# Kernel tuning notes

Measured on AMD Instinct MI355X. Metric: run time of the kernel, lower is better.

## Reference

```python
import jax, jax.numpy as jnp
import numpy as np

OUTPUT_DIM = 2
HIDDEN_DIM = 512
NUM_MODES = 6
PRED_LEN = 60
BATCH = 8192


def setup_inputs() -> dict:
    key = jax.random.key(0)
    ks = jax.random.split(key, 12)
    H, D, M = HIDDEN_DIM, OUTPUT_DIM, NUM_MODES
    s = 1.0 / np.sqrt(H)  # PyTorch default uniform(-1/sqrt(H), 1/sqrt(H))
    u = lambda k, shape: jax.random.uniform(k, shape, jnp.float32, -s, s)
    return {
        "social_features": jax.random.normal(ks[0], (BATCH, H), jnp.float32),
        "hidden": jax.random.normal(ks[1], (1, BATCH, H), jnp.float32),
        "cell": jax.random.normal(ks[2], (1, BATCH, H), jnp.float32),
        "w_ih": u(ks[3], (4 * H, D + H)),   # LSTM input->gates (i,f,g,o)
        "w_hh": u(ks[4], (4 * H, H)),       # LSTM hidden->gates
        "b_ih": u(ks[5], (4 * H,)),
        "b_hh": u(ks[6], (4 * H,)),
        "w_out": u(ks[7], (D * M, H)),      # output_layer
        "b_out": u(ks[8], (D * M,)),
        "w_mode": u(ks[9], (M, H)),         # mode_prob_layer
        "b_mode": u(ks[10], (M,)),
        "pred_len": PRED_LEN,
    }


def _decode(social_features, hidden, cell, w_ih, w_hh, b_ih, b_hh,
            w_out, b_out, w_mode, b_mode, pred_len):
    B = social_features.shape[0]
    H, D, M = HIDDEN_DIM, OUTPUT_DIM, NUM_MODES
    h0 = hidden[0]  # num_layers == 1
    c0 = cell[0]
    x0 = jnp.zeros((B, D), social_features.dtype)
    bias = b_ih + b_hh

    def step(carry, _):
        x, h, c = carry
        inp = jnp.concatenate([x, social_features], axis=-1)  # [B, D+H]
        gates = inp @ w_ih.T + h @ w_hh.T + bias              # [B, 4H]
        i, f, g, o = jnp.split(gates, 4, axis=-1)             # PyTorch gate order
        i = jax.nn.sigmoid(i)
        f = jax.nn.sigmoid(f)
        g = jnp.tanh(g)
        o = jax.nn.sigmoid(o)
        c_new = f * c + i * g
        h_new = o * jnp.tanh(c_new)
        pred = (h_new @ w_out.T + b_out).reshape(B, M, D)     # [B, M, D]
        mode_prob = jax.nn.softmax(h_new @ w_mode.T + b_mode, axis=-1)  # [B, M]
        x_next = pred[:, 0, :]
        return (x_next, h_new, c_new), (pred, mode_prob)

    _, (preds, probs) = jax.lax.scan(step, (x0, h0, c0), None, length=pred_len)
    # scan stacks on leading time axis -> move to batch-first
    predictions = jnp.transpose(preds, (1, 0, 2, 3))  # [B, T, M, D]
    mode_probs = jnp.transpose(probs, (1, 0, 2))      # [B, T, M]
    return predictions, mode_probs


def reference(social_features, hidden, cell, w_ih, w_hh, b_ih, b_hh,
              w_out, b_out, w_mode, b_mode, pred_len):
    return _decode(social_features, hidden, cell, w_ih, w_hh, b_ih, b_hh,
                   w_out, b_out, w_mode, b_mode, pred_len)
```

## Files before the change

kernel.cpp:

```cpp
#include <hip/hip_runtime.h>

#define H 512
#define BATCHN 8192
#define STEPS 60

#define WEFF_OFF   0u
#define WPLAIN_OFF 2097152u
#define WIHS_OFF   4194304u
#define WSM_OFF    6291456u
#define BSM_OFF    6324224u
#define BX1_OFF    6324352u
#define BX0_OFF    6332544u
#define HB0_OFF    8388608u
#define HB1_OFF    16777216u
#define CPACK_OFF  25165824u
#define SPACK_OFF  41943040u

typedef short s16x8 __attribute__((ext_vector_type(8)));
typedef float f32x4 __attribute__((ext_vector_type(4)));
typedef unsigned int u32x2 __attribute__((ext_vector_type(2)));
typedef unsigned int u32x4 __attribute__((ext_vector_type(4)));

__device__ inline unsigned f2bf(float f) {
  unsigned u = __builtin_bit_cast(unsigned, f);
  return (u + 0x7fffu + ((u >> 16) & 1u)) >> 16;
}
__device__ inline float bf2f(unsigned s) {
  return __builtin_bit_cast(float, s << 16);
}
__device__ inline float sigm(float x) {
  float e = __builtin_amdgcn_exp2f(-1.442695041f * x);
  return __builtin_amdgcn_rcpf(1.0f + e);
}
__device__ inline float tanh_(float x) {
  float e = __builtin_amdgcn_exp2f(2.885390082f * x);
  return 1.0f - 2.0f * __builtin_amdgcn_rcpf(1.0f + e);
}
__device__ inline f32x4 mfma16(s16x8 a, s16x8 b, f32x4 c) {
  return __builtin_amdgcn_mfma_f32_16x16x32_bf16(a, b, c, 0, 0, 0);
}
__device__ inline int haddr(int b, int k) {
  return b * 1024 + ((k * 2) ^ ((b & 7) << 4));
}

__global__ void pack_kernel(const float* __restrict__ w_ih, const float* __restrict__ w_hh,
                            const float* __restrict__ w_out, const float* __restrict__ b_out,
                            const float* __restrict__ w_mode, const float* __restrict__ b_mode,
                            unsigned char* __restrict__ ws) {
  unsigned idx = blockIdx.x * 256 + threadIdx.x;
  if (idx < 2097152u) {
    unsigned j = idx & 1048575u;
    bool eff = idx < 1048576u;
    unsigned e = j & 7u, lane = (j >> 3) & 63u, kb = (j >> 9) & 15u, T = j >> 13;
    unsigned i = lane & 15u;
    unsigned hcol = T * 4u + (i >> 2), gate = i & 3u;
    unsigned n = gate * 512u + hcol;
    unsigned k = kb * 32u + (lane >> 4) * 8u + e;
    float v = w_hh[(size_t)n * 512u + k];
    if (eff) v += w_ih[(size_t)n * 514u] * w_out[k] + w_ih[(size_t)n * 514u + 1u] * w_out[512u + k];
    ((unsigned short*)(ws + (eff ? WEFF_OFF : WPLAIN_OFF)))[j] = (unsigned short)f2bf(v);
  } else if (idx < 3145728u) {
    unsigned j = idx - 2097152u;
    unsigned e = j & 7u, lane = (j >> 3) & 63u, kb = (j >> 9) & 15u, nb = j >> 13;
    unsigned n = nb * 16u + (lane & 15u), k = kb * 32u + (lane >> 4) * 8u + e;
    ((unsigned short*)(ws + WIHS_OFF))[j] = (unsigned short)f2bf(w_ih[(size_t)n * 514u + 2u + k]);
  } else if (idx < 3162112u) {
    unsigned j = idx - 3145728u;
    unsigned e = j & 7u, lane = (j >> 3) & 63u, kb = (j >> 9) & 15u, nb = j >> 13;
    unsigned o = nb * 16u + (lane & 15u), k = kb * 32u + (lane >> 4) * 8u + e;
    float v = 0.0f;
    if (o < 12u) v = w_out[o * 512u + k];
    else if (o < 18u) v = w_mode[(o - 12u) * 512u + k];
    ((unsigned short*)(ws + WSM_OFF))[j] = (unsigned short)f2bf(v);
  } else if (idx < 3162144u) {
    unsigned o = idx - 3162112u;
    float v = 0.0f;
    if (o < 12u) v = b_out[o];
    else if (o < 18u) v = b_mode[o - 12u];
    ((float*)(ws + BSM_OFF))[o] = v;
  } else if (idx < 3164192u) {
    unsigned m = idx - 3162144u;
    unsigned T = m >> 4, i = m & 15u;
    unsigned hcol = T * 4u + (i >> 2), gate = i & 3u;
    unsigned n = gate * 512u + hcol;
    ((float*)(ws + BX1_OFF))[m] = w_ih[(size_t)n * 514u] * b_out[0] + w_ih[(size_t)n * 514u + 1u] * b_out[1];
  } else if (idx < 3166240u) {
    ((float*)(ws + BX0_OFF))[idx - 3164192u] = 0.0f;
  }
}

__global__ __launch_bounds__(512, 2) void prep_kernel(
    const float* __restrict__ social, const float* __restrict__ hidden,
    const float* __restrict__ cell, const float* __restrict__ b_ih,
    const float* __restrict__ b_hh, unsigned char* __restrict__ ws) {
  const int tid = threadIdx.x;
  const int wid = tid >> 6;
  const int lane = tid & 63;
  const int q = lane >> 4;
  const int r = lane & 15;
  const int wg = blockIdx.x;
  const int gb0 = wg * 32;

  const s16x8* wihs_w = (const s16x8*)(ws + WIHS_OFF) + (size_t)wid * 4096 + lane;
  unsigned short* spack = (unsigned short*)(ws + SPACK_OFF);
  unsigned short* hb0 = (unsigned short*)(ws + HB0_OFF);
  float* cpackp = (float*)(ws + CPACK_OFF);

  __shared__ unsigned short h_lds[32 * H];

  s16x8 wbuf[4][4];
  #pragma unroll
  for (int d = 0; d < 4; ++d)
    #pragma unroll
    for (int g = 0; g < 4; ++g)
      wbuf[d][g] = wihs_w[g * 32768 + d * 64];

  #pragma unroll
  for (int i = 0; i < 8; ++i) {
    int rr = i * 4 + (tid >> 7);
    int kk = (tid & 127) * 4;
    f32x4 v = *(const f32x4*)(social + (size_t)(gb0 + rr) * H + kk);
    u32x2 p;
    p[0] = f2bf(v[0]) | (f2bf(v[1]) << 16);
    p[1] = f2bf(v[2]) | (f2bf(v[3]) << 16);
    *(u32x2*)((char*)h_lds + haddr(rr, kk)) = p;
  }
  __syncthreads();

  #pragma unroll
  for (int jb = 0; jb < 4; ++jb) {
    f32x4 acc[4][2];
    #pragma unroll
    for (int g = 0; g < 4; ++g) {
      int n0 = g * 512 + wid * 64 + jb * 16 + q * 4;
      f32x4 bi = *(const f32x4*)(b_ih + n0);
      f32x4 bh = *(const f32x4*)(b_hh + n0);
      f32x4 bias = bi + bh;
      acc[g][0] = bias; acc[g][1] = bias;
    }
    #pragma unroll
    for (int kb = 0; kb < 16; ++kb) {
      const int F = jb * 16 + kb;
      const int slot = F & 3;
      s16x8 bfrag[2];
      #pragma unroll
      for (int bb = 0; bb < 2; ++bb)
        bfrag[bb] = *(const s16x8*)((char*)h_lds + haddr(bb * 16 + r, kb * 32 + q * 8));
      s16x8 af[4];
      #pragma unroll
      for (int g = 0; g < 4; ++g) af[g] = wbuf[slot][g];
      {
        const int Fn = (F + 4) & 63;
        const int jn = Fn >> 4, kn = Fn & 15;
        #pragma unroll
        for (int g = 0; g < 4; ++g)
          wbuf[slot][g] = wihs_w[g * 32768 + jn * 1024 + kn * 64];
      }
      #pragma unroll
      for (int g = 0; g < 4; ++g) {
        acc[g][0] = mfma16(af[g], bfrag[0], acc[g][0]);
        acc[g][1] = mfma16(af[g], bfrag[1], acc[g][1]);
      }
    }
    #pragma unroll
    for (int bb = 0; bb < 2; ++bb) {
      unsigned wrd[8];
      #pragma unroll
      for (int j = 0; j < 8; ++j) {
        int e = j >> 1, gp = (j & 1) * 2;
        wrd[j] = f2bf(acc[gp][bb][e]) | (f2bf(acc[gp + 1][bb][e]) << 16);
      }
      int T = wid * 16 + jb * 4 + q;
      int b = gb0 + bb * 16 + r;
      char* dst = (char*)spack + ((size_t)T * 8192 + b) * 32;
      u32x4 w0; w0[0] = wrd[0]; w0[1] = wrd[1]; w0[2] = wrd[2]; w0[3] = wrd[3];
      u32x4 w1; w1[0] = wrd[4]; w1[1] = wrd[5]; w1[2] = wrd[6]; w1[3] = wrd[7];
      *(u32x4*)dst = w0;
      *(u32x4*)(dst + 16) = w1;
    }
  }

  {
    const float* hsrc = hidden + (size_t)gb0 * H;
    unsigned short* hdst = hb0 + (size_t)gb0 * H;
    int base = tid * 32;
    #pragma unroll
    for (int v8 = 0; v8 < 4; ++v8) {
      f32x4 x0 = *(const f32x4*)(hsrc + base + v8 * 8);
      f32x4 x1 = *(const f32x4*)(hsrc + base + v8 * 8 + 4);
      u32x4 pk;
      pk[0] = f2bf(x0[0]) | (f2bf(x0[1]) << 16);
      pk[1] = f2bf(x0[2]) | (f2bf(x0[3]) << 16);
      pk[2] = f2bf(x1[0]) | (f2bf(x1[1]) << 16);
      pk[3] = f2bf(x1[2]) | (f2bf(x1[3]) << 16);
      *(u32x4*)(hdst + base + v8 * 8) = pk;
    }
  }

  for (int j = 0; j < 32; ++j) {
    int flat = tid * 32 + j;
    int b = gb0 + (flat >> 9);
    int hcol = flat & 511;
    float v = cell[(size_t)b * 512 + hcol];
    int jg2 = hcol >> 6, w2 = (hcol >> 3) & 7, Tl = (hcol >> 2) & 1, q2 = hcol & 3;
    int bg2 = b >> 8, ib2 = (b >> 4) & 15, r2 = b & 15;
    int wg2 = jg2 * 32 + bg2;
    cpackp[(((size_t)(wg2 * 8 + w2) * 16 + ib2) * 2 + Tl) * 64 + q2 * 16 + r2] = v;
  }
}

__device__ inline void stage_load(const unsigned short* h_in, int b0, int p, int tid,
                                  s16x8 sreg[4]) {
  #pragma unroll
  for (int i = 0; i < 4; ++i) {
    int f = tid * 64 + i * 16;
    int row = f >> 10, off = f & 1023;
    sreg[i] = *(const s16x8*)((const char*)h_in + (size_t)(b0 + p * 32 + row) * 1024 + off);
  }
}
__device__ inline void stage_write(unsigned short* buf, int tid, const s16x8 sreg[4]) {
  #pragma unroll
  for (int i = 0; i < 4; ++i) {
    int f = tid * 64 + i * 16;
    int row = f >> 10, off = f & 1023;
    *(s16x8*)((char*)buf + row * 1024 + (off ^ ((row & 7) << 4))) = sreg[i];
  }
}

__global__ __launch_bounds__(512, 2) void step_kernel(
    const s16x8* __restrict__ whh, const float* __restrict__ bx,
    const unsigned short* __restrict__ spack, const s16x8* __restrict__ wsm,
    const float* __restrict__ bsm, const unsigned short* __restrict__ h_in,
    unsigned short* __restrict__ h_out, float* __restrict__ cpack,
    float* __restrict__ out, int tprev) {
  const int tid = threadIdx.x;
  const int wid = tid >> 6;
  const int lane = tid & 63;
  const int q = lane >> 4;
  const int r = lane & 15;
  const int wg = blockIdx.x;
  const int jg = wg >> 5;
  const int bg = wg & 31;
  const int b0 = bg * 256;
  const size_t MODE_BASE = (size_t)BATCHN * 720;

  __shared__ s16x8 wsm_lds[2048];
  __shared__ unsigned short hinA[32 * 512];
  __shared__ unsigned short hinB[32 * 512];
  __shared__ unsigned short hout_lds[256 * 64];
  __shared__ float mode_lds[8][16][8];

  s16x8 A0[16], A1[16];
  #pragma unroll
  for (int kb = 0; kb < 16; ++kb) {
    A0[kb] = whh[(size_t)((jg * 16 + wid * 2 + 0) * 16 + kb) * 64 + lane];
    A1[kb] = whh[(size_t)((jg * 16 + wid * 2 + 1) * 16 + kb) * 64 + lane];
  }
  float creg[16][2];
  #pragma unroll
  for (int ib = 0; ib < 16; ++ib) {
    creg[ib][0] = cpack[(size_t)(((wg * 8 + wid) * 16 + ib) * 2 + 0) * 64 + lane];
    creg[ib][1] = cpack[(size_t)(((wg * 8 + wid) * 16 + ib) * 2 + 1) * 64 + lane];
  }
  f32x4 bxv0 = *(const f32x4*)(bx + (jg * 16 + wid * 2 + 0) * 16 + q * 4);
  f32x4 bxv1 = *(const f32x4*)(bx + (jg * 16 + wid * 2 + 1) * 16 + q * 4);
  f32x4 pb0 = *(const f32x4*)(bsm + q * 4);
  f32x4 pb1 = *(const f32x4*)(bsm + 16 + q * 4);
  #pragma unroll
  for (int i = 0; i < 4; ++i) wsm_lds[i * 512 + tid] = wsm[i * 512 + tid];

  s16x8 sreg[4];
  stage_load(h_in, b0, 0, tid, sreg);
  stage_write(hinA, tid, sreg);
  stage_load(h_in, b0, 1, tid, sreg);
  __syncthreads();

  #pragma unroll
  for (int rr = 0; rr < 8; ++rr) {
    if (rr < 7) {
      unsigned short* wb = ((rr + 1) & 1) ? hinB : hinA;
      stage_write(wb, tid, sreg);
      if (rr < 6) stage_load(h_in, b0, rr + 2, tid, sreg);
    }
    const unsigned short* hbuf = (rr & 1) ? hinB : hinA;
    const bool dop = (wid == rr) && (tprev >= 0);
    #pragma unroll
    for (int ib2 = 0; ib2 < 2; ++ib2) {
      const int bt = rr * 2 + ib2;
      const int b = b0 + bt * 16 + r;
      u32x2 sv0 = *(const u32x2*)((const char*)spack +
                    ((size_t)(jg * 16 + wid * 2 + 0) * 8192 + b) * 32 + q * 8);
      u32x2 sv1 = *(const u32x2*)((const char*)spack +
                    ((size_t)(jg * 16 + wid * 2 + 1) * 8192 + b) * 32 + q * 8);
      f32x4 acc0, acc1;
      acc0[0] = bf2f(sv0[0] & 0xffffu) + bxv0[0];
      acc0[1] = bf2f(sv0[0] >> 16)     + bxv0[1];
      acc0[2] = bf2f(sv0[1] & 0xffffu) + bxv0[2];
      acc0[3] = bf2f(sv0[1] >> 16)     + bxv0[3];
      acc1[0] = bf2f(sv1[0] & 0xffffu) + bxv1[0];
      acc1[1] = bf2f(sv1[0] >> 16)     + bxv1[1];
      acc1[2] = bf2f(sv1[1] & 0xffffu) + bxv1[2];
      acc1[3] = bf2f(sv1[1] >> 16)     + bxv1[3];
      #pragma unroll
      for (int kb = 0; kb < 16; ++kb) {
        s16x8 bfrag = *(const s16x8*)((const char*)hbuf + (ib2 * 16 + r) * 1024 +
                        ((kb * 64 + q * 16) ^ ((r & 7) << 4)));
        acc0 = mfma16(A0[kb], bfrag, acc0);
        acc1 = mfma16(A1[kb], bfrag, acc1);
      }
      #pragma unroll
      for (int Tl = 0; Tl < 2; ++Tl) {
        f32x4 ac = Tl ? acc1 : acc0;
        float iv = sigm(ac[0]), fv = sigm(ac[1]), gv = tanh_(ac[2]), ov = sigm(ac[3]);
        float cn = fv * creg[bt][Tl] + iv * gv;
        creg[bt][Tl] = cn;
        float hn = ov * tanh_(cn);
        int col = wid * 8 + Tl * 4 + q;
        int row = bt * 16 + r;
        *(unsigned short*)((char*)hout_lds + row * 128 + ((col * 2) ^ ((r & 7) << 4))) =
            (unsigned short)f2bf(hn);
      }
      if (dop) {
        f32x4 p0 = pb0, p1 = pb1;
        #pragma unroll
        for (int kb = 0; kb < 16; ++kb) {
          s16x8 bfrag = *(const s16x8*)((const char*)hbuf + (ib2 * 16 + r) * 1024 +
                          ((kb * 64 + q * 16) ^ ((r & 7) << 4)));
          p0 = mfma16(wsm_lds[kb * 64 + lane], bfrag, p0);
          p1 = mfma16(wsm_lds[(16 + kb) * 64 + lane], bfrag, p1);
        }
        if (q < 3) *(f32x4*)(out + ((size_t)b * 60 + tprev) * 12 + q * 4) = p0;
        if (q == 3) *(f32x4*)(&mode_lds[wid][r][0]) = p0;
        if (q == 0) { mode_lds[wid][r][4] = p1[0]; mode_lds[wid][r][5] = p1[1]; }
        if (q == 1) {
          float v0 = mode_lds[wid][r][0], v1 = mode_lds[wid][r][1], v2 = mode_lds[wid][r][2];
          float v3 = mode_lds[wid][r][3], v4 = mode_lds[wid][r][4], v5 = mode_lds[wid][r][5];
          float mx = fmaxf(fmaxf(fmaxf(v0, v1), fmaxf(v2, v3)), fmaxf(v4, v5));
          float e0 = __builtin_amdgcn_exp2f(1.442695041f * (v0 - mx));
          float e1 = __builtin_amdgcn_exp2f(1.442695041f * (v1 - mx));
          float e2 = __builtin_amdgcn_exp2f(1.442695041f * (v2 - mx));
          float e3 = __builtin_amdgcn_exp2f(1.442695041f * (v3 - mx));
          float e4 = __builtin_amdgcn_exp2f(1.442695041f * (v4 - mx));
          float e5 = __builtin_amdgcn_exp2f(1.442695041f * (v5 - mx));
          float s = e0 + e1 + e2 + e3 + e4 + e5;
          float inv = __builtin_amdgcn_rcpf(s);
          float* mo = out + MODE_BASE + (size_t)b * 360 + tprev * 6;
          mo[0] = e0 * inv; mo[1] = e1 * inv; mo[2] = e2 * inv;
          mo[3] = e3 * inv; mo[4] = e4 * inv; mo[5] = e5 * inv;
        }
      }
    }
    __syncthreads();
  }

  #pragma unroll
  for (int i = 0; i < 4; ++i) {
    int f = tid * 64 + i * 16;
    int row = f >> 7, off = f & 127;
    s16x8 v = *(const s16x8*)((const char*)hout_lds + row * 128 + (off ^ ((row & 7) << 4)));
    *(s16x8*)((char*)h_out + (size_t)(b0 + row) * 1024 + jg * 128 + off) = v;
  }
  #pragma unroll
  for (int ib = 0; ib < 16; ++ib) {
    cpack[(size_t)(((wg * 8 + wid) * 16 + ib) * 2 + 0) * 64 + lane] = creg[ib][0];
    cpack[(size_t)(((wg * 8 + wid) * 16 + ib) * 2 + 1) * 64 + lane] = creg[ib][1];
  }
}

__global__ __launch_bounds__(256) void projf_kernel(
    const unsigned short* __restrict__ h_in, const s16x8* __restrict__ wsm,
    const float* __restrict__ bsm, float* __restrict__ out) {
  const int tid = threadIdx.x;
  const int wid = tid >> 6;
  const int lane = tid & 63;
  const int q = lane >> 4;
  const int r = lane & 15;
  const int wg = blockIdx.x;
  const int b0 = wg * 32;
  const int bt = wid & 1, T = wid >> 1;
  const size_t MODE_BASE = (size_t)BATCHN * 720;
  __shared__ float mbuf[32][8];

  f32x4 pacc = *(const f32x4*)(bsm + T * 16 + q * 4);
  #pragma unroll
  for (int kb = 0; kb < 16; ++kb) {
    s16x8 bfrag = *(const s16x8*)((const char*)h_in +
                    (size_t)(b0 + bt * 16 + r) * 1024 + kb * 64 + q * 16);
    s16x8 af = wsm[(T * 16 + kb) * 64 + lane];
    pacc = mfma16(af, bfrag, pacc);
  }
  int b = b0 + bt * 16 + r;
  if (T == 0) {
    if (q < 3) *(f32x4*)(out + ((size_t)b * 60 + 59) * 12 + q * 4) = pacc;
    if (q == 3) *(f32x4*)(&mbuf[bt * 16 + r][0]) = pacc;
  } else {
    if (q == 0) { mbuf[bt * 16 + r][4] = pacc[0]; mbuf[bt * 16 + r][5] = pacc[1]; }
  }
  __syncthreads();
  if (tid < 32) {
    float v0 = mbuf[tid][0], v1 = mbuf[tid][1], v2 = mbuf[tid][2];
    float v3 = mbuf[tid][3], v4 = mbuf[tid][4], v5 = mbuf[tid][5];
    float mx = fmaxf(fmaxf(fmaxf(v0, v1), fmaxf(v2, v3)), fmaxf(v4, v5));
    float e0 = __builtin_amdgcn_exp2f(1.442695041f * (v0 - mx));
    float e1 = __builtin_amdgcn_exp2f(1.442695041f * (v1 - mx));
    float e2 = __builtin_amdgcn_exp2f(1.442695041f * (v2 - mx));
    float e3 = __builtin_amdgcn_exp2f(1.442695041f * (v3 - mx));
    float e4 = __builtin_amdgcn_exp2f(1.442695041f * (v4 - mx));
    float e5 = __builtin_amdgcn_exp2f(1.442695041f * (v5 - mx));
    float s = e0 + e1 + e2 + e3 + e4 + e5;
    float inv = __builtin_amdgcn_rcpf(s);
    float* mo = out + MODE_BASE + (size_t)(b0 + tid) * 360 + 59 * 6;
    mo[0] = e0 * inv; mo[1] = e1 * inv; mo[2] = e2 * inv;
    mo[3] = e3 * inv; mo[4] = e4 * inv; mo[5] = e5 * inv;
  }
}

extern "C" void kernel_launch(void* const* d_in, const int* in_sizes, int n_in,
                              void* d_out, int out_size, void* d_ws, size_t ws_size,
                              hipStream_t stream) {
  const float* social = (const float*)d_in[0];
  const float* hidden = (const float*)d_in[1];
  const float* cell   = (const float*)d_in[2];
  const float* w_ih   = (const float*)d_in[3];
  const float* w_hh   = (const float*)d_in[4];
  const float* b_ih   = (const float*)d_in[5];
  const float* b_hh   = (const float*)d_in[6];
  const float* w_out  = (const float*)d_in[7];
  const float* b_out  = (const float*)d_in[8];
  const float* w_mode = (const float*)d_in[9];
  const float* b_mode = (const float*)d_in[10];
  unsigned char* ws = (unsigned char*)d_ws;
  float* out = (float*)d_out;

  hipLaunchKernelGGL(pack_kernel, dim3((3166240u + 255u) / 256u), dim3(256), 0, stream,
                     w_ih, w_hh, w_out, b_out, w_mode, b_mode, ws);
  hipLaunchKernelGGL(prep_kernel, dim3(256), dim3(512), 0, stream,
                     social, hidden, cell, b_ih, b_hh, ws);

  const s16x8* weff   = (const s16x8*)(ws + WEFF_OFF);
  const s16x8* wplain = (const s16x8*)(ws + WPLAIN_OFF);
  const s16x8* wsm    = (const s16x8*)(ws + WSM_OFF);
  const float* bsm    = (const float*)(ws + BSM_OFF);
  const float* bx1    = (const float*)(ws + BX1_OFF);
  const float* bx0    = (const float*)(ws + BX0_OFF);
  const unsigned short* spack = (const unsigned short*)(ws + SPACK_OFF);
  unsigned short* hb[2] = {(unsigned short*)(ws + HB0_OFF), (unsigned short*)(ws + HB1_OFF)};
  float* cpack = (float*)(ws + CPACK_OFF);

  for (int s = 0; s < STEPS; ++s) {
    hipLaunchKernelGGL(step_kernel, dim3(256), dim3(512), 0, stream,
                       (s == 0) ? wplain : weff, (s == 0) ? bx0 : bx1,
                       spack, wsm, bsm, hb[s & 1], hb[(s + 1) & 1], cpack, out, s - 1);
  }
  hipLaunchKernelGGL(projf_kernel, dim3(256), dim3(256), 0, stream,
                     hb[0], wsm, bsm, out);
}
```

Before: 4.503 ms.

## Fuse per-step LSTM launches into one persistent cooperative kernel with grid sync

Replaces the 60 separate step_kernel launches with a single cooperative kernel that loops over time steps and separates them with a grid-wide sync. Weights, cell state and biases stay in registers across steps, so they are no longer reloaded and the cell state is no longer written back every step. The social-feature loads are also prefetched one tile ahead. In exchange it relies on all 256 workgroups being co-resident and pays a grid barrier per step. The bx0 bias is replaced by a zero vector at step 0.

```diff
diff --git a/kernel.cpp b/kernel.cpp
--- a/kernel.cpp
+++ b/kernel.cpp
@@ -1,4 +1,7 @@
 #include <hip/hip_runtime.h>
+#include <hip/hip_cooperative_groups.h>
+
+namespace cg = cooperative_groups;
 
 #define H 512
 #define BATCHN 8192
@@ -227,12 +230,13 @@
   }
 }
 
-__global__ __launch_bounds__(512, 2) void step_kernel(
-    const s16x8* __restrict__ whh, const float* __restrict__ bx,
-    const unsigned short* __restrict__ spack, const s16x8* __restrict__ wsm,
-    const float* __restrict__ bsm, const unsigned short* __restrict__ h_in,
-    unsigned short* __restrict__ h_out, float* __restrict__ cpack,
-    float* __restrict__ out, int tprev) {
+__global__ __launch_bounds__(512, 2) void coop_kernel(
+    const s16x8* __restrict__ weff, const s16x8* __restrict__ wplain,
+    const float* __restrict__ bx, const unsigned short* __restrict__ spack,
+    const s16x8* __restrict__ wsm, const float* __restrict__ bsm,
+    unsigned short* __restrict__ hb0, unsigned short* __restrict__ hb1,
+    const float* __restrict__ cpack, float* __restrict__ out) {
+  cg::grid_group gridg = cg::this_grid();
   const int tid = threadIdx.x;
   const int wid = tid >> 6;
   const int lane = tid & 63;
@@ -253,8 +257,8 @@
   s16x8 A0[16], A1[16];
   #pragma unroll
   for (int kb = 0; kb < 16; ++kb) {
-    A0[kb] = whh[(size_t)((jg * 16 + wid * 2 + 0) * 16 + kb) * 64 + lane];
-    A1[kb] = whh[(size_t)((jg * 16 + wid * 2 + 1) * 16 + kb) * 64 + lane];
+    A0[kb] = wplain[(size_t)((jg * 16 + wid * 2 + 0) * 16 + kb) * 64 + lane];
+    A1[kb] = wplain[(size_t)((jg * 16 + wid * 2 + 1) * 16 + kb) * 64 + lane];
   }
   float creg[16][2];
   #pragma unroll
@@ -262,108 +266,127 @@
     creg[ib][0] = cpack[(size_t)(((wg * 8 + wid) * 16 + ib) * 2 + 0) * 64 + lane];
     creg[ib][1] = cpack[(size_t)(((wg * 8 + wid) * 16 + ib) * 2 + 1) * 64 + lane];
   }
-  f32x4 bxv0 = *(const f32x4*)(bx + (jg * 16 + wid * 2 + 0) * 16 + q * 4);
-  f32x4 bxv1 = *(const f32x4*)(bx + (jg * 16 + wid * 2 + 1) * 16 + q * 4);
-  f32x4 pb0 = *(const f32x4*)(bsm + q * 4);
-  f32x4 pb1 = *(const f32x4*)(bsm + 16 + q * 4);
+  const f32x4 bxv0 = *(const f32x4*)(bx + (jg * 16 + wid * 2 + 0) * 16 + q * 4);
+  const f32x4 bxv1 = *(const f32x4*)(bx + (jg * 16 + wid * 2 + 1) * 16 + q * 4);
+  const f32x4 pb0 = *(const f32x4*)(bsm + q * 4);
+  const f32x4 pb1 = *(const f32x4*)(bsm + 16 + q * 4);
   #pragma unroll
   for (int i = 0; i < 4; ++i) wsm_lds[i * 512 + tid] = wsm[i * 512 + tid];
 
-  s16x8 sreg[4];
-  stage_load(h_in, b0, 0, tid, sreg);
-  stage_write(hinA, tid, sreg);
-  stage_load(h_in, b0, 1, tid, sreg);
-  __syncthreads();
-
-  #pragma unroll
-  for (int rr = 0; rr < 8; ++rr) {
-    if (rr < 7) {
-      unsigned short* wb = ((rr + 1) & 1) ? hinB : hinA;
-      stage_write(wb, tid, sreg);
-      if (rr < 6) stage_load(h_in, b0, rr + 2, tid, sreg);
-    }
-    const unsigned short* hbuf = (rr & 1) ? hinB : hinA;
-    const bool dop = (wid == rr) && (tprev >= 0);
-    #pragma unroll
-    for (int ib2 = 0; ib2 < 2; ++ib2) {
-      const int bt = rr * 2 + ib2;
-      const int b = b0 + bt * 16 + r;
-      u32x2 sv0 = *(const u32x2*)((const char*)spack +
-                    ((size_t)(jg * 16 + wid * 2 + 0) * 8192 + b) * 32 + q * 8);
-      u32x2 sv1 = *(const u32x2*)((const char*)spack +
-                    ((size_t)(jg * 16 + wid * 2 + 1) * 8192 + b) * 32 + q * 8);
-      f32x4 acc0, acc1;
-      acc0[0] = bf2f(sv0[0] & 0xffffu) + bxv0[0];
-      acc0[1] = bf2f(sv0[0] >> 16)     + bxv0[1];
-      acc0[2] = bf2f(sv0[1] & 0xffffu) + bxv0[2];
-      acc0[3] = bf2f(sv0[1] >> 16)     + bxv0[3];
-      acc1[0] = bf2f(sv1[0] & 0xffffu) + bxv1[0];
-      acc1[1] = bf2f(sv1[0] >> 16)     + bxv1[1];
-      acc1[2] = bf2f(sv1[1] & 0xffffu) + bxv1[2];
-      acc1[3] = bf2f(sv1[1] >> 16)     + bxv1[3];
-      #pragma unroll
-      for (int kb = 0; kb < 16; ++kb) {
-        s16x8 bfrag = *(const s16x8*)((const char*)hbuf + (ib2 * 16 + r) * 1024 +
-                        ((kb * 64 + q * 16) ^ ((r & 7) << 4)));
-        acc0 = mfma16(A0[kb], bfrag, acc0);
-        acc1 = mfma16(A1[kb], bfrag, acc1);
-      }
-      #pragma unroll
-      for (int Tl = 0; Tl < 2; ++Tl) {
-        f32x4 ac = Tl ? acc1 : acc0;
-        float iv = sigm(ac[0]), fv = sigm(ac[1]), gv = tanh_(ac[2]), ov = sigm(ac[3]);
-        float cn = fv * creg[bt][Tl] + iv * gv;
-        creg[bt][Tl] = cn;
-        float hn = ov * tanh_(cn);
-        int col = wid * 8 + Tl * 4 + q;
-        int row = bt * 16 + r;
-        *(unsigned short*)((char*)hout_lds + row * 128 + ((col * 2) ^ ((r & 7) << 4))) =
-            (unsigned short)f2bf(hn);
-      }
-      if (dop) {
-        f32x4 p0 = pb0, p1 = pb1;
+  const char* sp0 = (const char*)spack + ((size_t)(jg * 16 + wid * 2 + 0) * 8192) * 32 + q * 8;
+  const char* sp1 = (const char*)spack + ((size_t)(jg * 16 + wid * 2 + 1) * 8192) * 32 + q * 8;
+
+  #pragma unroll 1
+  for (int s = 0; s < STEPS; ++s) {
+    const unsigned short* h_in = (s & 1) ? hb1 : hb0;
+    unsigned short* h_out = (s & 1) ? hb0 : hb1;
+    const f32x4 zero = {0.0f, 0.0f, 0.0f, 0.0f};
+    const f32x4 bz0 = (s == 0) ? zero : bxv0;
+    const f32x4 bz1 = (s == 0) ? zero : bxv1;
+
+    s16x8 sreg[4];
+    stage_load(h_in, b0, 0, tid, sreg);
+    stage_write(hinA, tid, sreg);
+    stage_load(h_in, b0, 1, tid, sreg);
+    u32x2 sv0 = *(const u32x2*)(sp0 + (size_t)(b0 + r) * 32);
+    u32x2 sv1 = *(const u32x2*)(sp1 + (size_t)(b0 + r) * 32);
+    __syncthreads();
+
+    #pragma unroll
+    for (int rr = 0; rr < 8; ++rr) {
+      if (rr < 7) {
+        unsigned short* wb = ((rr + 1) & 1) ? hinB : hinA;
+        stage_write(wb, tid, sreg);
+        if (rr < 6) stage_load(h_in, b0, rr + 2, tid, sreg);
+      }
+      const unsigned short* hbuf = (rr & 1) ? hinB : hinA;
+      const bool dop = (wid == rr) && (s > 0);
+      #pragma unroll
+      for (int ib2 = 0; ib2 < 2; ++ib2) {
+        const int bt = rr * 2 + ib2;
+        const int b = b0 + bt * 16 + r;
+        u32x2 cs0 = sv0, cs1 = sv1;
+        if (bt < 15) {
+          sv0 = *(const u32x2*)(sp0 + (size_t)(b + 16) * 32);
+          sv1 = *(const u32x2*)(sp1 + (size_t)(b + 16) * 32);
+        }
+        f32x4 acc0, acc1;
+        acc0[0] = bf2f(cs0[0] & 0xffffu) + bz0[0];
+        acc0[1] = bf2f(cs0[0] >> 16)     + bz0[1];
+        acc0[2] = bf2f(cs0[1] & 0xffffu) + bz0[2];
+        acc0[3] = bf2f(cs0[1] >> 16)     + bz0[3];
+        acc1[0] = bf2f(cs1[0] & 0xffffu) + bz1[0];
+        acc1[1] = bf2f(cs1[0] >> 16)     + bz1[1];
+        acc1[2] = bf2f(cs1[1] & 0xffffu) + bz1[2];
+        acc1[3] = bf2f(cs1[1] >> 16)     + bz1[3];
         #pragma unroll
         for (int kb = 0; kb < 16; ++kb) {
           s16x8 bfrag = *(const s16x8*)((const char*)hbuf + (ib2 * 16 + r) * 1024 +
                           ((kb * 64 + q * 16) ^ ((r & 7) << 4)));
-          p0 = mfma16(wsm_lds[kb * 64 + lane], bfrag, p0);
-          p1 = mfma16(wsm_lds[(16 + kb) * 64 + lane], bfrag, p1);
+          acc0 = mfma16(A0[kb], bfrag, acc0);
+          acc1 = mfma16(A1[kb], bfrag, acc1);
         }
-        if (q < 3) *(f32x4*)(out + ((size_t)b * 60 + tprev) * 12 + q * 4) = p0;
-        if (q == 3) *(f32x4*)(&mode_lds[wid][r][0]) = p0;
-        if (q == 0) { mode_lds[wid][r][4] = p1[0]; mode_lds[wid][r][5] = p1[1]; }
-        if (q == 1) {
-          float v0 = mode_lds[wid][r][0], v1 = mode_lds[wid][r][1], v2 = mode_lds[wid][r][2];
-          float v3 = mode_lds[wid][r][3], v4 = mode_lds[wid][r][4], v5 = mode_lds[wid][r][5];
-          float mx = fmaxf(fmaxf(fmaxf(v0, v1), fmaxf(v2, v3)), fmaxf(v4, v5));
-          float e0 = __builtin_amdgcn_exp2f(1.442695041f * (v0 - mx));
-          float e1 = __builtin_amdgcn_exp2f(1.442695041f * (v1 - mx));
-          float e2 = __builtin_amdgcn_exp2f(1.442695041f * (v2 - mx));
-          float e3 = __builtin_amdgcn_exp2f(1.442695041f * (v3 - mx));
-          float e4 = __builtin_amdgcn_exp2f(1.442695041f * (v4 - mx));
-          float e5 = __builtin_amdgcn_exp2f(1.442695041f * (v5 - mx));
-          float s = e0 + e1 + e2 + e3 + e4 + e5;
-          float inv = __builtin_amdgcn_rcpf(s);
-          float* mo = out + MODE_BASE + (size_t)b * 360 + tprev * 6;
-          mo[0] = e0 * inv; mo[1] = e1 * inv; mo[2] = e2 * inv;
-          mo[3] = e3 * inv; mo[4] = e4 * inv; mo[5] = e5 * inv;
+        #pragma unroll
+        for (int Tl = 0; Tl < 2; ++Tl) {
+          f32x4 ac = Tl ? acc1 : acc0;
+          float iv = sigm(ac[0]), fv = sigm(ac[1]), gv = tanh_(ac[2]), ov = sigm(ac[3]);
+          float cn = fv * creg[bt][Tl] + iv * gv;
+          creg[bt][Tl] = cn;
+          float hn = ov * tanh_(cn);
+          int col = wid * 8 + Tl * 4 + q;
+          int row = bt * 16 + r;
+          *(unsigned short*)((char*)hout_lds + row * 128 + ((col * 2) ^ ((r & 7) << 4))) =
+              (unsigned short)f2bf(hn);
         }
-      }
-    }
-    __syncthreads();
-  }
-
-  #pragma unroll
-  for (int i = 0; i < 4; ++i) {
-    int f = tid * 64 + i * 16;
-    int row = f >> 7, off = f & 127;
-    s16x8 v = *(const s16x8*)((const char*)hout_lds + row * 128 + (off ^ ((row & 7) << 4)));
-    *(s16x8*)((char*)h_out + (size_t)(b0 + row) * 1024 + jg * 128 + off) = v;
-  }
-  #pragma unroll
-  for (int ib = 0; ib < 16; ++ib) {
-    cpack[(size_t)(((wg * 8 + wid) * 16 + ib) * 2 + 0) * 64 + lane] = creg[ib][0];
-    cpack[(size_t)(((wg * 8 + wid) * 16 + ib) * 2 + 1) * 64 + lane] = creg[ib][1];
+        if (dop) {
+          const int tprev = s - 1;
+          f32x4 p0 = pb0, p1 = pb1;
+          #pragma unroll
+          for (int kb = 0; kb < 16; ++kb) {
+            s16x8 bfrag = *(const s16x8*)((const char*)hbuf + (ib2 * 16 + r) * 1024 +
+                            ((kb * 64 + q * 16) ^ ((r & 7) << 4)));
+            p0 = mfma16(wsm_lds[kb * 64 + lane], bfrag, p0);
+            p1 = mfma16(wsm_lds[(16 + kb) * 64 + lane], bfrag, p1);
+          }
+          if (q < 3) *(f32x4*)(out + ((size_t)b * 60 + tprev) * 12 + q * 4) = p0;
+          if (q == 3) *(f32x4*)(&mode_lds[wid][r][0]) = p0;
+          if (q == 0) { mode_lds[wid][r][4] = p1[0]; mode_lds[wid][r][5] = p1[1]; }
+          if (q == 1) {
+            float v0 = mode_lds[wid][r][0], v1 = mode_lds[wid][r][1], v2 = mode_lds[wid][r][2];
+            float v3 = mode_lds[wid][r][3], v4 = mode_lds[wid][r][4], v5 = mode_lds[wid][r][5];
+            float mx = fmaxf(fmaxf(fmaxf(v0, v1), fmaxf(v2, v3)), fmaxf(v4, v5));
+            float e0 = __builtin_amdgcn_exp2f(1.442695041f * (v0 - mx));
+            float e1 = __builtin_amdgcn_exp2f(1.442695041f * (v1 - mx));
+            float e2 = __builtin_amdgcn_exp2f(1.442695041f * (v2 - mx));
+            float e3 = __builtin_amdgcn_exp2f(1.442695041f * (v3 - mx));
+            float e4 = __builtin_amdgcn_exp2f(1.442695041f * (v4 - mx));
+            float e5 = __builtin_amdgcn_exp2f(1.442695041f * (v5 - mx));
+            float su = e0 + e1 + e2 + e3 + e4 + e5;
+            float inv = __builtin_amdgcn_rcpf(su);
+            float* mo = out + MODE_BASE + (size_t)b * 360 + tprev * 6;
+            mo[0] = e0 * inv; mo[1] = e1 * inv; mo[2] = e2 * inv;
+            mo[3] = e3 * inv; mo[4] = e4 * inv; mo[5] = e5 * inv;
+          }
+        }
+      }
+      __syncthreads();
+    }
+    #pragma unroll
+    for (int i = 0; i < 4; ++i) {
+      int f = tid * 64 + i * 16;
+      int row = f >> 7, off = f & 127;
+      s16x8 v = *(const s16x8*)((const char*)hout_lds + row * 128 + (off ^ ((row & 7) << 4)));
+      *(s16x8*)((char*)h_out + (size_t)(b0 + row) * 1024 + jg * 128 + off) = v;
+    }
+    __threadfence();
+    gridg.sync();
+    if (s == 0) {
+      #pragma unroll
+      for (int kb = 0; kb < 16; ++kb) {
+        A0[kb] = weff[(size_t)((jg * 16 + wid * 2 + 0) * 16 + kb) * 64 + lane];
+        A1[kb] = weff[(size_t)((jg * 16 + wid * 2 + 1) * 16 + kb) * 64 + lane];
+      }
+    }
   }
 }
 
@@ -442,16 +465,17 @@
   const s16x8* wsm    = (const s16x8*)(ws + WSM_OFF);
   const float* bsm    = (const float*)(ws + BSM_OFF);
   const float* bx1    = (const float*)(ws + BX1_OFF);
-  const float* bx0    = (const float*)(ws + BX0_OFF);
   const unsigned short* spack = (const unsigned short*)(ws + SPACK_OFF);
-  unsigned short* hb[2] = {(unsigned short*)(ws + HB0_OFF), (unsigned short*)(ws + HB1_OFF)};
-  float* cpack = (float*)(ws + CPACK_OFF);
-
-  for (int s = 0; s < STEPS; ++s) {
-    hipLaunchKernelGGL(step_kernel, dim3(256), dim3(512), 0, stream,
-                       (s == 0) ? wplain : weff, (s == 0) ? bx0 : bx1,
-                       spack, wsm, bsm, hb[s & 1], hb[(s + 1) & 1], cpack, out, s - 1);
-  }
+  unsigned short* hb0p = (unsigned short*)(ws + HB0_OFF);
+  unsigned short* hb1p = (unsigned short*)(ws + HB1_OFF);
+  const float* cpackc = (const float*)(ws + CPACK_OFF);
+
+  void* args[] = {(void*)&weff, (void*)&wplain, (void*)&bx1, (void*)&spack,
+                  (void*)&wsm, (void*)&bsm, (void*)&hb0p, (void*)&hb1p,
+                  (void*)&cpackc, (void*)&out};
+  hipLaunchCooperativeKernel((const void*)coop_kernel, dim3(256), dim3(512),
+                             args, 0, stream);
+
   hipLaunchKernelGGL(projf_kernel, dim3(256), dim3(256), 0, stream,
-                     hb[0], wsm, bsm, out);
-}
+                     hb0p, wsm, bsm, out);
+}
```

Measured after the change: 9.491 ms. 111% more time.
